# Kernel optimization log

Hardware: AMD Instinct MI355X
Metric: run time of the kernel (lower is better)

Reference implementation:

```python
import jax, jax.numpy as jnp
import numpy as np


def setup_inputs() -> dict:
    key = jax.random.key(0)
    k1, k2, k3 = jax.random.split(key, 3)
    N, K, d, d_out = 100000, 32, 64, 64
    x = jax.random.normal(k1, (N, d), dtype=jnp.float32)
    edge_index = jax.random.randint(k2, (N, K), 0, N, dtype=jnp.int64)
    W = jax.random.normal(k3, (2 * d, d_out), dtype=jnp.float32) * (1.0 / np.sqrt(2 * d))
    b = jnp.zeros((d_out,), dtype=jnp.float32)
    return {"x": x, "edge_index": edge_index, "W": W, "b": b}


def reference(x, edge_index, W, b):
    # x: [N, d], edge_index: [N, K] dense neighbor indices
    x_j = x[edge_index]                                  # [N, K, d] gather
    # concat([x_i, x_j - x_i]) then max over K. The x_i half is constant over K,
    # so its max is x itself; max of the diff half computed directly (same math,
    # avoids materializing the [N, K, 2d] concat).
    diff_max = jnp.max(x_j - x[:, None, :], axis=1)      # [N, d]
    h = jnp.concatenate([x, diff_max], axis=-1)          # [N, 2d]
    return h @ W + b                                     # [N, d_out]
```

## Files before the change

kernel.cpp:

```cpp
#include <hip/hip_runtime.h>
#include <hip/hip_bf16.h>
#include <cstdint>


typedef __attribute__((ext_vector_type(8))) short short8;
typedef __attribute__((ext_vector_type(4))) float f4;

#define TILE 16
#define ROWS 168
#define EIS  34
#define BIAS 8.0f

__device__ __forceinline__ unsigned short f2bf(float f) {
  unsigned int u = __builtin_bit_cast(unsigned int, f);
  u += 0x7fffu + ((u >> 16) & 1u);
  return (unsigned short)(u >> 16);
}
__device__ __forceinline__ unsigned int pack2(float a, float b) {
  return (unsigned int)f2bf(a) | ((unsigned int)f2bf(b) << 16);
}
__device__ __forceinline__ float bflo(unsigned int u) {
  return __builtin_bit_cast(float, u << 16);
}
__device__ __forceinline__ float bfhi(unsigned int u) {
  return __builtin_bit_cast(float, u & 0xffff0000u);
}
__device__ __forceinline__ unsigned int pkmax(unsigned int a, unsigned int b) {
  unsigned int d;
  asm("v_pk_max_u16 %0, %1, %2" : "=v"(d) : "v"(a), "v"(b));
  return d;
}

__global__ __launch_bounds__(256)
void convert_kernel(const float* __restrict__ x, unsigned int* __restrict__ xbfB,
                    const float* __restrict__ W, unsigned short* __restrict__ wf,
                    int n8, int nxb) {
  if ((int)blockIdx.x < nxb) {
    int i = blockIdx.x * 256 + threadIdx.x;
    if (i >= n8) return;
    const f4* p = (const f4*)x + (size_t)i * 2;
    f4 a = p[0], b = p[1];
    uint4 w;
    w.x = pack2(a.x + BIAS, a.y + BIAS); w.y = pack2(a.z + BIAS, a.w + BIAS);
    w.z = pack2(b.x + BIAS, b.y + BIAS); w.w = pack2(b.z + BIAS, b.w + BIAS);
    ((uint4*)xbfB)[i] = w;
  } else {
    #pragma unroll
    for (int q = 0; q < 4; ++q) {
      int idx = threadIdx.x * 4 + q;
      int wv = idx >> 8, ks = (idx >> 6) & 3, l = idx & 63;
      int c = l & 15, g = l >> 4;
      short8 v;
      #pragma unroll
      for (int j = 0; j < 8; ++j)
        v[j] = (short)f2bf(W[(ks * 32 + g * 8 + j) * 64 + wv * 16 + c]);
      *(short8*)(wf + (size_t)idx * 8) = v;
    }
  }
}

__global__ __launch_bounds__(256, 6)
void mrconv4_kernel(const float* __restrict__ x,
                    const unsigned int* __restrict__ xbfB,
                    const unsigned short* __restrict__ wf,
                    const int* __restrict__ ei,
                    const float* __restrict__ bias,
                    float* __restrict__ out,
                    int n_tiles)
{
  __shared__ __align__(16) unsigned short hs[TILE * ROWS];
  __shared__ __align__(16) int eis[TILE * EIS];
  __shared__ __align__(16) float otile[TILE * 64];

  const int tid  = threadIdx.x;
  const int wv   = tid >> 6;
  const int lane = tid & 63;
  const int c = lane & 15;
  const int g = lane >> 4;
  const int t2 = lane >> 4;
  const int h  = (lane >> 3) & 1;
  const int e  = lane & 7;

  const int node0 = blockIdx.x * TILE;
  const int t = wv * 4 + t2;

  {
    int row = tid >> 4;
    int col = (tid & 15) * 2;
    *(int2*)&eis[row * EIS + col] = *(const int2*)(ei + (size_t)node0 * 32 + tid * 2);
  }
  __syncthreads();

  const unsigned int* gbase = xbfB + e * 4;
  const int ebase = t * EIS + h;
  uint4 macc = {0u, 0u, 0u, 0u};
  #pragma unroll
  for (int half = 0; half < 2; ++half) {
    uint4 r[8];
    #pragma unroll
    for (int i = 0; i < 8; ++i) {
      const int j = eis[ebase + half * 16 + i * 2];
      r[i] = *(const uint4*)(gbase + (size_t)j * 32);
    }
    #pragma unroll
    for (int i = 0; i < 8; ++i) {
      macc.x = pkmax(macc.x, r[i].x);
      macc.y = pkmax(macc.y, r[i].y);
      macc.z = pkmax(macc.z, r[i].z);
      macc.w = pkmax(macc.w, r[i].w);
    }
  }

  short8 bfrag[4];
  #pragma unroll
  for (int ks = 0; ks < 4; ++ks)
    bfrag[ks] = *(const short8*)(wf + (size_t)((wv * 4 + ks) * 64 + lane) * 8);

  macc.x = pkmax(macc.x, __shfl_xor(macc.x, 8));
  macc.y = pkmax(macc.y, __shfl_xor(macc.y, 8));
  macc.z = pkmax(macc.z, __shfl_xor(macc.z, 8));
  macc.w = pkmax(macc.w, __shfl_xor(macc.w, 8));

  if (h == 0) {
    const uint4 xrb = *(const uint4*)(xbfB + (size_t)(node0 + t) * 32 + e * 4);
    uint4 w;
    w.x = pack2(bflo(macc.x) - bflo(xrb.x), bfhi(macc.x) - bfhi(xrb.x));
    w.y = pack2(bflo(macc.y) - bflo(xrb.y), bfhi(macc.y) - bfhi(xrb.y));
    w.z = pack2(bflo(macc.z) - bflo(xrb.z), bfhi(macc.z) - bfhi(xrb.z));
    w.w = pack2(bflo(macc.w) - bflo(xrb.w), bfhi(macc.w) - bfhi(xrb.w));
    *(uint4*)(hs + t * ROWS + 64 + e * 8) = w;
  } else {
    const f4 xa = *(const f4*)(x + (size_t)(node0 + t) * 64 + e * 8);
    const f4 xb = *(const f4*)(x + (size_t)(node0 + t) * 64 + e * 8 + 4);
    uint4 w;
    w.x = pack2(xa.x, xa.y); w.y = pack2(xa.z, xa.w);
    w.z = pack2(xb.x, xb.y); w.w = pack2(xb.z, xb.w);
    *(uint4*)(hs + t * ROWS + e * 8) = w;
  }
  __syncthreads();

  f4 acc = {0.f, 0.f, 0.f, 0.f};
  #pragma unroll
  for (int ks = 0; ks < 4; ++ks) {
    short8 a = *(const short8*)(hs + c * ROWS + ks * 32 + g * 8);
    acc = __builtin_amdgcn_mfma_f32_16x16x32_bf16(a, bfrag[ks], acc, 0, 0, 0);
  }

  const float bb = bias[wv * 16 + c];
  #pragma unroll
  for (int j = 0; j < 4; ++j)
    otile[(g * 4 + j) * 64 + wv * 16 + c] = acc[j] + bb;
  __syncthreads();
  *(f4*)(out + (size_t)node0 * 64 + tid * 4) = *(const f4*)&otile[tid * 4];
}

#define FWPB 4
#define FROWS 160
__global__ __launch_bounds__(256, 4)
void mrconv_fp32_kernel(const float* __restrict__ x,
                        const int* __restrict__ ei,
                        const float* __restrict__ W,
                        const float* __restrict__ bias,
                        float* __restrict__ out,
                        int n_tiles)
{
  __shared__ __align__(16) unsigned short hsf[FWPB][TILE * FROWS];
  const int wave = threadIdx.x >> 6;
  const int lane = threadIdx.x & 63;
  const int c = lane & 15;
  const int g = lane >> 4;

  short8 bfrag[4][4];
  #pragma unroll
  for (int ks = 0; ks < 4; ++ks) {
    #pragma unroll
    for (int nt = 0; nt < 4; ++nt) {
      short8 v;
      #pragma unroll
      for (int j = 0; j < 8; ++j) {
        int k = ks * 32 + g * 8 + j;
        v[j] = (short)f2bf(W[k * 64 + nt * 16 + c]);
      }
      bfrag[ks][nt] = v;
    }
  }

  const int tile = blockIdx.x * FWPB + wave;
  if (tile >= n_tiles) return;
  const int node0 = tile * TILE;
  unsigned short* hrow = &hsf[wave][0];

  #pragma unroll 2
  for (int t = 0; t < TILE; ++t) {
    const int n = node0 + t;
    const f4 xi = *(const f4*)(x + (size_t)n * 64 + 4 * c);
    f4 m = { -3.4e38f, -3.4e38f, -3.4e38f, -3.4e38f };
    #pragma unroll
    for (int it = 0; it < 8; ++it) {
      const int j = ei[(size_t)n * 32 + it * 4 + g];
      const f4 xj = *(const f4*)(x + (size_t)j * 64 + 4 * c);
      m.x = fmaxf(m.x, xj.x - xi.x);
      m.y = fmaxf(m.y, xj.y - xi.y);
      m.z = fmaxf(m.z, xj.z - xi.z);
      m.w = fmaxf(m.w, xj.w - xi.w);
    }
    m.x = fmaxf(m.x, __shfl_xor(m.x, 16));
    m.y = fmaxf(m.y, __shfl_xor(m.y, 16));
    m.z = fmaxf(m.z, __shfl_xor(m.z, 16));
    m.w = fmaxf(m.w, __shfl_xor(m.w, 16));
    m.x = fmaxf(m.x, __shfl_xor(m.x, 32));
    m.y = fmaxf(m.y, __shfl_xor(m.y, 32));
    m.z = fmaxf(m.z, __shfl_xor(m.z, 32));
    m.w = fmaxf(m.w, __shfl_xor(m.w, 32));
    if (g == 0) {
      ushort4 p;
      p.x = f2bf(xi.x); p.y = f2bf(xi.y); p.z = f2bf(xi.z); p.w = f2bf(xi.w);
      *(ushort4*)(hrow + t * FROWS + 4 * c) = p;
    } else if (g == 1) {
      ushort4 p;
      p.x = f2bf(m.x); p.y = f2bf(m.y); p.z = f2bf(m.z); p.w = f2bf(m.w);
      *(ushort4*)(hrow + t * FROWS + 64 + 4 * c) = p;
    }
  }
  __asm__ volatile("s_waitcnt lgkmcnt(0)" ::: "memory");

  f4 acc[4] = {{0.f,0.f,0.f,0.f},{0.f,0.f,0.f,0.f},{0.f,0.f,0.f,0.f},{0.f,0.f,0.f,0.f}};
  #pragma unroll
  for (int ks = 0; ks < 4; ++ks) {
    short8 a = *(const short8*)(hrow + c * FROWS + ks * 32 + g * 8);
    #pragma unroll
    for (int nt = 0; nt < 4; ++nt)
      acc[nt] = __builtin_amdgcn_mfma_f32_16x16x32_bf16(a, bfrag[ks][nt], acc[nt], 0, 0, 0);
  }
  const int rbase = node0 + g * 4;
  #pragma unroll
  for (int nt = 0; nt < 4; ++nt) {
    const float bb = bias[nt * 16 + c];
    #pragma unroll
    for (int j = 0; j < 4; ++j)
      out[(size_t)(rbase + j) * 64 + nt * 16 + c] = acc[nt][j] + bb;
  }
}

extern "C" void kernel_launch(void* const* d_in, const int* in_sizes, int n_in,
                              void* d_out, int out_size, void* d_ws, size_t ws_size,
                              hipStream_t stream) {
  const float* x  = (const float*)d_in[0];
  const int*   ei = (const int*)d_in[1];
  const float* W  = (const float*)d_in[2];
  const float* b  = (const float*)d_in[3];
  float* out = (float*)d_out;

  const int N = in_sizes[0] / 64;
  const int n_tiles = N / TILE;

  const size_t xbf_bytes = (size_t)N * 64 * 2;
  const size_t wf_bytes  = 1024 * 16;
  if (ws_size >= xbf_bytes + wf_bytes) {
    unsigned int*   xbfB = (unsigned int*)d_ws;
    unsigned short* wf   = (unsigned short*)((char*)d_ws + xbf_bytes);
    const int n8  = N * 64 / 8;
    const int nxb = (n8 + 255) / 256;
    hipLaunchKernelGGL(convert_kernel, dim3(nxb + 1), dim3(256), 0, stream,
                       x, xbfB, W, wf, n8, nxb);
    hipLaunchKernelGGL(mrconv4_kernel, dim3(n_tiles), dim3(256), 0, stream,
                       x, xbfB, wf, ei, b, out, n_tiles);
  } else {
    const int blocks = (n_tiles + FWPB - 1) / FWPB;
    hipLaunchKernelGGL(mrconv_fp32_kernel, dim3(blocks), dim3(256), 0, stream,
                       x, ei, W, b, out, n_tiles);
  }
}
```

Baseline: 135.8 us.

## Load neighbor indices directly to registers and issue all 16 gathers at once

Removes the shared-memory staging of edge indices and its block barrier: each lane now reads its 16 neighbor indices straight from global memory with vector loads. It then issues all 16 gather loads before reducing them in a tree of packed max operations, and loads the node's own features early so they overlap with the gathers. The goal is more memory-level parallelism per wave. The cost is higher register pressure, reflected in the occupancy hint dropping from 6 to 4 blocks per CU, and some redundant index loads across lanes.

```diff
diff --git a/kernel.cpp b/kernel.cpp
--- a/kernel.cpp
+++ b/kernel.cpp
@@ -8,7 +8,6 @@
 
 #define TILE 16
 #define ROWS 168
-#define EIS  34
 #define BIAS 8.0f
 
 __device__ __forceinline__ unsigned short f2bf(float f) {
@@ -28,6 +27,12 @@
 __device__ __forceinline__ unsigned int pkmax(unsigned int a, unsigned int b) {
   unsigned int d;
   asm("v_pk_max_u16 %0, %1, %2" : "=v"(d) : "v"(a), "v"(b));
+  return d;
+}
+__device__ __forceinline__ uint4 pkmax4(uint4 a, uint4 b) {
+  uint4 d;
+  d.x = pkmax(a.x, b.x); d.y = pkmax(a.y, b.y);
+  d.z = pkmax(a.z, b.z); d.w = pkmax(a.w, b.w);
   return d;
 }
 
@@ -59,8 +64,8 @@
   }
 }
 
-__global__ __launch_bounds__(256, 6)
-void mrconv4_kernel(const float* __restrict__ x,
+__global__ __launch_bounds__(256, 4)
+void mrconv5_kernel(const float* __restrict__ x,
                     const unsigned int* __restrict__ xbfB,
                     const unsigned short* __restrict__ wf,
                     const int* __restrict__ ei,
@@ -69,7 +74,6 @@
                     int n_tiles)
 {
   __shared__ __align__(16) unsigned short hs[TILE * ROWS];
-  __shared__ __align__(16) int eis[TILE * EIS];
   __shared__ __align__(16) float otile[TILE * 64];
 
   const int tid  = threadIdx.x;
@@ -83,33 +87,39 @@
 
   const int node0 = blockIdx.x * TILE;
   const int t = wv * 4 + t2;
-
-  {
-    int row = tid >> 4;
-    int col = (tid & 15) * 2;
-    *(int2*)&eis[row * EIS + col] = *(const int2*)(ei + (size_t)node0 * 32 + tid * 2);
-  }
-  __syncthreads();
-
-  const unsigned int* gbase = xbfB + e * 4;
-  const int ebase = t * EIS + h;
-  uint4 macc = {0u, 0u, 0u, 0u};
-  #pragma unroll
-  for (int half = 0; half < 2; ++half) {
-    uint4 r[8];
-    #pragma unroll
-    for (int i = 0; i < 8; ++i) {
-      const int j = eis[ebase + half * 16 + i * 2];
-      r[i] = *(const uint4*)(gbase + (size_t)j * 32);
-    }
-    #pragma unroll
-    for (int i = 0; i < 8; ++i) {
-      macc.x = pkmax(macc.x, r[i].x);
-      macc.y = pkmax(macc.y, r[i].y);
-      macc.z = pkmax(macc.z, r[i].z);
-      macc.w = pkmax(macc.w, r[i].w);
-    }
-  }
+  const int n = node0 + t;
+
+  uint4 xrb = {0u,0u,0u,0u};
+  f4 xa = {0.f,0.f,0.f,0.f}, xb = {0.f,0.f,0.f,0.f};
+  if (h == 0) {
+    xrb = *(const uint4*)(xbfB + (size_t)n * 32 + e * 4);
+  } else {
+    xa = *(const f4*)(x + (size_t)n * 64 + e * 8);
+    xb = *(const f4*)(x + (size_t)n * 64 + e * 8 + 4);
+  }
+
+  const int* eib = ei + (size_t)n * 32 + h * 16;
+  int4 i0 = *(const int4*)(eib + 0);
+  int4 i1 = *(const int4*)(eib + 4);
+  int4 i2 = *(const int4*)(eib + 8);
+  int4 i3 = *(const int4*)(eib + 12);
+  int jj[16] = {i0.x, i0.y, i0.z, i0.w, i1.x, i1.y, i1.z, i1.w,
+                i2.x, i2.y, i2.z, i2.w, i3.x, i3.y, i3.z, i3.w};
+
+  const char* gbase = (const char*)xbfB + (e << 4);
+  uint4 r[16];
+  #pragma unroll
+  for (int i = 0; i < 16; ++i)
+    r[i] = *(const uint4*)(gbase + ((size_t)(unsigned)jj[i] << 7));
+
+  uint4 m8[8];
+  #pragma unroll
+  for (int i = 0; i < 8; ++i) m8[i] = pkmax4(r[2 * i], r[2 * i + 1]);
+  uint4 m4[4];
+  #pragma unroll
+  for (int i = 0; i < 4; ++i) m4[i] = pkmax4(m8[2 * i], m8[2 * i + 1]);
+  uint4 m2a = pkmax4(m4[0], m4[1]), m2b = pkmax4(m4[2], m4[3]);
+  uint4 macc = pkmax4(m2a, m2b);
 
   short8 bfrag[4];
   #pragma unroll
@@ -122,7 +132,6 @@
   macc.w = pkmax(macc.w, __shfl_xor(macc.w, 8));
 
   if (h == 0) {
-    const uint4 xrb = *(const uint4*)(xbfB + (size_t)(node0 + t) * 32 + e * 4);
     uint4 w;
     w.x = pack2(bflo(macc.x) - bflo(xrb.x), bfhi(macc.x) - bfhi(xrb.x));
     w.y = pack2(bflo(macc.y) - bflo(xrb.y), bfhi(macc.y) - bfhi(xrb.y));
@@ -130,8 +139,6 @@
     w.w = pack2(bflo(macc.w) - bflo(xrb.w), bfhi(macc.w) - bfhi(xrb.w));
     *(uint4*)(hs + t * ROWS + 64 + e * 8) = w;
   } else {
-    const f4 xa = *(const f4*)(x + (size_t)(node0 + t) * 64 + e * 8);
-    const f4 xb = *(const f4*)(x + (size_t)(node0 + t) * 64 + e * 8 + 4);
     uint4 w;
     w.x = pack2(xa.x, xa.y); w.y = pack2(xa.z, xa.w);
     w.z = pack2(xb.x, xb.y); w.w = pack2(xb.z, xb.w);
@@ -263,7 +270,7 @@
     const int nxb = (n8 + 255) / 256;
     hipLaunchKernelGGL(convert_kernel, dim3(nxb + 1), dim3(256), 0, stream,
                        x, xbfB, W, wf, n8, nxb);
-    hipLaunchKernelGGL(mrconv4_kernel, dim3(n_tiles), dim3(256), 0, stream,
+    hipLaunchKernelGGL(mrconv5_kernel, dim3(n_tiles), dim3(256), 0, stream,
                        x, xbfB, wf, ei, b, out, n_tiles);
   } else {
     const int blocks = (n_tiles + FWPB - 1) / FWPB;
```

Result: no change. 136.0 us (+0.1%).
